# Kernel tuning notes

Hardware: AMD Instinct MI355X
Metric: run time of the kernel (lower is better)

## Reference

```python
import jax, jax.numpy as jnp
import numpy as np

B, S, D, H = 4, 1024, 1024, 16
DK = D // H
BLEND = 0.5
NEG = -1000000000.0


def setup_inputs() -> dict:
    key = jax.random.key(0)
    ks = jax.random.split(key, 16)
    scale = 0.02
    inp = {
        'query': jax.random.normal(ks[0], (B, S, D), jnp.float32),
        'key': jax.random.normal(ks[1], (B, S, D), jnp.float32),
        'value': jax.random.normal(ks[2], (B, S, D), jnp.float32),
        'relation_matrix': jax.random.uniform(ks[3], (B, H, S, S), jnp.float32),
        'Wq': jax.random.normal(ks[4], (D, D), jnp.float32) * scale,
        'bq': jnp.zeros((D,), jnp.float32),
        'Wk': jax.random.normal(ks[5], (D, D), jnp.float32) * scale,
        'bk': jnp.zeros((D,), jnp.float32),
        'Wv': jax.random.normal(ks[6], (D, D), jnp.float32) * scale,
        'bv': jnp.zeros((D,), jnp.float32),
        'Wo': jax.random.normal(ks[7], (D, D), jnp.float32) * scale,
        'bo': jnp.zeros((D,), jnp.float32),
        'mask': jnp.ones((B, 1, S, S), jnp.bool_),
        'padding_mask': jax.random.randint(ks[8], (B, S), 0, 2).astype(jnp.bool_),
    }
    return inp


def _split_heads(x):
    # [B,S,D] -> [B,H,S,DK]
    return x.reshape(B, S, H, DK).transpose(0, 2, 1, 3)


def reference(query, key, value, relation_matrix, Wq, bq, Wk, bk, Wv, bv, Wo, bo, mask, padding_mask):
    q = _split_heads(query @ Wq.T + bq)
    k = _split_heads(key @ Wk.T + bk)
    v = _split_heads(value @ Wv.T + bv)
    # mask * padding_mask (bool AND), broadcast to [B,H,S,S]
    full_mask = mask & padding_mask[:, None, None, :]
    scores = jnp.einsum('bhqd,bhkd->bhqk', q, k) / jnp.sqrt(jnp.float32(DK))
    scores = jnp.where(full_mask, scores, NEG)
    p = jax.nn.softmax(scores, axis=-1)
    p = jnp.where(jnp.isnan(p), jnp.zeros_like(p), p)
    p = BLEND * p + (1.0 - BLEND) * relation_matrix
    p = jnp.where(full_mask, p, 0.0)
    # dropout p=0 -> identity
    x = jnp.einsum('bhqk,bhkd->bhqd', p, v)
    x = x.transpose(0, 2, 1, 3).reshape(B, S, D)
    return x @ Wo.T + bo
```

## Files before the change

kernel.cpp:

```cpp
#include <hip/hip_runtime.h>
#include <hip/hip_bf16.h>

#define B_ 4
#define S_ 1024
#define D_ 1024
#define H_ 16
#define DK_ 64

typedef __attribute__((ext_vector_type(8))) short short8;
typedef __attribute__((ext_vector_type(4))) float f32x4;
typedef unsigned long long ull;

union U16x8 { uint4 q; short8 s; unsigned short h[8]; };

__device__ __forceinline__ unsigned short f2bf(float f) {
  union { float f; unsigned u; } a; a.f = f;
  unsigned u = a.u;
  u += 0x7FFF + ((u >> 16) & 1);
  return (unsigned short)(u >> 16);
}

__device__ __forceinline__ void gload_lds16(const void* g, void* l) {
  __builtin_amdgcn_global_load_lds(
      (const __attribute__((address_space(1))) unsigned int*)g,
      (__attribute__((address_space(3))) unsigned int*)l, 16, 0, 0);
}

__device__ __forceinline__ void fence_sched() {
  asm volatile("" ::: "memory");
}
__device__ __forceinline__ void bar() {
  fence_sched();
  __builtin_amdgcn_s_barrier();
  fence_sched();
}

__global__ void k_prep(const float* __restrict__ q, const float* __restrict__ k,
                       const float* __restrict__ v,
                       const float* __restrict__ Wq, const float* __restrict__ Wk,
                       const float* __restrict__ Wv, const float* __restrict__ Wo,
                       unsigned short* __restrict__ Aq, unsigned short* __restrict__ Ak,
                       unsigned short* __restrict__ Av,
                       unsigned short* __restrict__ WqB, unsigned short* __restrict__ WkB,
                       unsigned short* __restrict__ WvB, unsigned short* __restrict__ WoB,
                       const unsigned char* __restrict__ padraw,
                       ull* __restrict__ qmW) {
  __shared__ unsigned char pl[4096];
  const int b = blockIdx.x, t = threadIdx.x;
  if (b == 8192) {
    bool nonzero_off = false, sawf = false;
    for (int i = 0; i < 128; ++i) {
      unsigned char c = padraw[i];
      if ((i & 3) && c) nonzero_off = true;
      if (c == 0x3F || c == 0x80) sawf = true;
    }
    int fmt = sawf ? 2 : (nonzero_off ? 0 : 1);
    for (int j = 0; j < 16; ++j) {
      int i = t * 16 + j;
      unsigned char val;
      if (fmt == 0)      val = padraw[i] != 0;
      else if (fmt == 1) val = padraw[(size_t)i * 4] != 0;
      else               val = ((const float*)padraw)[i] != 0.f;
      pl[i] = val;
    }
    __syncthreads();
    if (t < 64) {
      int bb = t >> 4, c = t & 15;
      ull m = 0;
      for (int j = 0; j < 64; ++j) m |= (ull)(pl[bb * 1024 + j * 16 + c] & 1) << j;
      qmW[t] = m;
    }
    return;
  }
  const float* src; unsigned short* dst; size_t base;
  if (b < 2048)      { src = q; dst = Aq; base = (size_t)b * 2048; }
  else if (b < 4096) { src = k; dst = Ak; base = (size_t)(b - 2048) * 2048; }
  else if (b < 6144) { src = v; dst = Av; base = (size_t)(b - 4096) * 2048; }
  else {
    int w = (b - 6144) >> 9, bb = (b - 6144) & 511;
    src = w == 0 ? Wq : w == 1 ? Wk : w == 2 ? Wv : Wo;
    dst = w == 0 ? WqB : w == 1 ? WkB : w == 2 ? WvB : WoB;
    base = (size_t)bb * 2048;
  }
  size_t i = base + (size_t)t * 8;
  float4 a = *(const float4*)(src + i);
  float4 c = *(const float4*)(src + i + 4);
  U16x8 o;
  o.h[0]=f2bf(a.x); o.h[1]=f2bf(a.y); o.h[2]=f2bf(a.z); o.h[3]=f2bf(a.w);
  o.h[4]=f2bf(c.x); o.h[5]=f2bf(c.y); o.h[6]=f2bf(c.z); o.h[7]=f2bf(c.w);
  *(uint4*)(dst + i) = o.q;
}

#define BM 128
#define BN 128
#define BKG 64
__global__ __launch_bounds__(256) void k_gemm(
    const unsigned short* __restrict__ A0, const unsigned short* __restrict__ A1,
    const unsigned short* __restrict__ A2,
    const unsigned short* __restrict__ W0, const unsigned short* __restrict__ W1,
    const unsigned short* __restrict__ W2,
    const float* __restrict__ bi0, const float* __restrict__ bi1, const float* __restrict__ bi2,
    void* __restrict__ C0, void* __restrict__ C1, void* __restrict__ C2,
    const ull* __restrict__ qm, int modeSel) {
  __shared__ unsigned short As[2][BM * BKG];
  __shared__ unsigned short Bs[2][BN * BKG];
  const int d0 = blockIdx.x;
  const int chunk = gridDim.x >> 3;
  const int o = (d0 & 7) * chunk + (d0 >> 3);
  const int z = o >> 8;
  const unsigned short* A  = z == 0 ? A0 : z == 1 ? A1 : A2;
  const unsigned short* Bw = z == 0 ? W0 : z == 1 ? W1 : W2;
  const float* bias        = z == 0 ? bi0 : z == 1 ? bi1 : bi2;
  void* Cout               = z == 0 ? C0 : z == 1 ? C1 : C2;
  const int mode = (modeSel == 2) ? 2 : (z == 2 ? 1 : 0);
  const int t = threadIdx.x;
  const int lane = t & 63;
  const int wid = t >> 6;
  const int wm = wid >> 1, wn = wid & 1;
  const int m0 = ((o >> 3) & 31) * BM, n0 = (o & 7) * BN;
  f32x4 acc[4][4] = {};

  auto stage = [&](int kt, int buf) {
    const int k0 = kt * BKG;
    char* AsB = (char*)As[buf]; char* BsB = (char*)Bs[buf];
#pragma unroll
    for (int i = 0; i < 4; ++i) {
      int lx = (t + i * 256) * 16;
      int row = lx >> 7;
      int colb = (lx & 127) ^ ((row & 7) << 4);
      gload_lds16((const char*)A + (size_t)(m0 + row) * (D_ * 2) + k0 * 2 + colb, AsB + lx);
    }
#pragma unroll
    for (int i = 0; i < 4; ++i) {
      int lx = (t + i * 256) * 16;
      int row = lx >> 7;
      int colb = (lx & 127) ^ ((row & 7) << 4);
      gload_lds16((const char*)Bw + (size_t)(n0 + row) * (D_ * 2) + k0 * 2 + colb, BsB + lx);
    }
  };

  asm volatile("s_waitcnt vmcnt(0)" ::: "memory");
  stage(0, 0);
#pragma unroll 1
  for (int kt = 0; kt < D_ / BKG; ++kt) {
    const int cur = kt & 1;
    if (kt < 15) {
      stage(kt + 1, cur ^ 1);
      asm volatile("s_waitcnt vmcnt(8)" ::: "memory");
    } else {
      asm volatile("s_waitcnt vmcnt(0)" ::: "memory");
    }
    __builtin_amdgcn_sched_barrier(0);
    bar();
    char* AsB = (char*)As[cur]; char* BsB = (char*)Bs[cur];
#pragma unroll
    for (int ks = 0; ks < 2; ++ks) {
      short8 aF[4], bF[4];
      int kbyte = ks * 64 + ((lane >> 4) << 4);
#pragma unroll
      for (int m = 0; m < 4; ++m) {
        int row = wm * 64 + m * 16 + (lane & 15);
        U16x8 u; u.q = *(const uint4*)(AsB + row * 128 + (kbyte ^ ((row & 7) << 4)));
        aF[m] = u.s;
      }
#pragma unroll
      for (int n = 0; n < 4; ++n) {
        int row = wn * 64 + n * 16 + (lane & 15);
        U16x8 u; u.q = *(const uint4*)(BsB + row * 128 + (kbyte ^ ((row & 7) << 4)));
        bF[n] = u.s;
      }
#pragma unroll
      for (int m = 0; m < 4; ++m)
#pragma unroll
        for (int n = 0; n < 4; ++n)
          acc[m][n] = __builtin_amdgcn_mfma_f32_16x16x32_bf16(aF[m], bF[n], acc[m][n], 0, 0, 0);
    }
    bar();
  }
#pragma unroll
  for (int m = 0; m < 4; ++m) {
#pragma unroll
    for (int n = 0; n < 4; ++n) {
#pragma unroll
      for (int r = 0; r < 4; ++r) {
        int rg = m0 + wm * 64 + m * 16 + ((lane >> 4) << 2) + r;
        int cg = n0 + wn * 64 + n * 16 + (lane & 15);
        float val = acc[m][n][r] + bias[cg];
        int bb = rg >> 10, s = rg & 1023;
        int hh = cg >> 6, dk = cg & 63;
        if (mode == 0)
          ((unsigned short*)Cout)[((size_t)(bb * H_ + hh) * S_ + s) * DK_ + dk] = f2bf(val);
        else if (mode == 1) {
          float pv = (float)((qm[bb * 16 + (s & 15)] >> (s >> 4)) & 1);
          val *= pv;
          ((unsigned short*)Cout)[((size_t)(bb * H_ + hh) * DK_ + dk) * S_ + s] = f2bf(val);
        } else
          ((float*)Cout)[(size_t)rg * D_ + cg] = val;
      }
    }
  }
}

__global__ __launch_bounds__(256) void k_attn(const unsigned short* __restrict__ Qh,
    const unsigned short* __restrict__ Kh, const unsigned short* __restrict__ Vt,
    const float* __restrict__ rel, const ull* __restrict__ qm,
    unsigned short* __restrict__ Xout) {
  __shared__ unsigned short Ks[2][4096];
  __shared__ unsigned short Vs[2][4096];
  __shared__ float Rl[2][4096];
  __shared__ unsigned short Pl[4096];
  const int t = threadIdx.x, lane = t & 63, wid = t >> 6;
  const int d0 = blockIdx.x;
  const int o = (d0 & 7) * 128 + (d0 >> 3);
  const int qt = o & 15, h = (o >> 4) & 15, b = o >> 8;
  const int bh = b * H_ + h;
  const int c = lane & 15, g = lane >> 4;
  const int q0 = qt * 64 + wid * 16;
  char* PlB = (char*)Pl + wid * 2048;

  ull qmask = qm[b * 16 + c];

  short8 qa[2];
#pragma unroll
  for (int ks = 0; ks < 2; ++ks) {
    U16x8 u;
    u.q = *(const uint4*)((const char*)Qh +
          ((size_t)(bh * S_ + q0 + c) * DK_ + ks * 32 + (g << 3)) * 2);
    qa[ks] = u.s;
  }
  f32x4 eacc[4] = {}, racc[4] = {};
  float Lp[4] = {0.f, 0.f, 0.f, 0.f};

  const char* relblk = (const char*)rel + ((size_t)(bh * S_ + qt * 64) * S_) * 4;
  auto stage = [&](int kt, int buf) {
    const int k0 = kt * 64;
    char* KsB = (char*)Ks[buf];
    char* VsB = (char*)Vs[buf];
    char* RlB = (char*)Rl[buf];
#pragma unroll
    for (int i = 0; i < 2; ++i) {
      int lx = (t + i * 256) * 16;
      int row = lx >> 7;
      int colb = (lx & 127) ^ ((row & 7) << 4);
      gload_lds16((const char*)Kh + ((size_t)(bh * S_ + k0 + row) * DK_) * 2 + colb, KsB + lx);
    }
#pragma unroll
    for (int i = 0; i < 2; ++i) {
      int lx = (t + i * 256) * 16;
      int row = lx >> 7;
      int colb = (lx & 127) ^ ((row & 7) << 4);
      gload_lds16((const char*)Vt + ((size_t)(bh * DK_ + row) * S_ + k0) * 2 + colb, VsB + lx);
    }
#pragma unroll
    for (int i = 0; i < 4; ++i) {
      int lx = t * 16 + i * 4096;
      int row = lx >> 8;
      int inner = (lx & 255) ^ ((row & 7) << 4);
      gload_lds16(relblk + (size_t)row * (S_ * 4) + (size_t)kt * 256 + inner, RlB + lx);
    }
  };

  asm volatile("s_waitcnt vmcnt(0)" ::: "memory");
  stage(0, 0);

#pragma unroll 1
  for (int kt = 0; kt < 16; ++kt) {
    const int cur = kt & 1;
    if (kt < 15) {
      stage(kt + 1, cur ^ 1);
      asm volatile("s_waitcnt vmcnt(8)" ::: "memory");
    } else {
      asm volatile("s_waitcnt vmcnt(0)" ::: "memory");
    }
    __builtin_amdgcn_sched_barrier(0);
    bar();
    char* KsB = (char*)Ks[cur]; char* VsB = (char*)Vs[cur];
    const char* RlB = (const char*)Rl[cur];
#pragma unroll
    for (int kb = 0; kb < 4; ++kb) {
      f32x4 sacc = {};
#pragma unroll
      for (int ks = 0; ks < 2; ++ks) {
        int row = kb * 16 + c;
        int kbyte = ks * 64 + (g << 4);
        U16x8 u; u.q = *(const uint4*)(KsB + row * 128 + (kbyte ^ ((row & 7) << 4)));
        sacc = __builtin_amdgcn_mfma_f32_16x16x32_bf16(qa[ks], u.s, sacc, 0, 0, 0);
      }
      float pv = ((qmask >> (kt * 4 + kb)) & 1) ? 1.0f : 0.0f;
#pragma unroll
      for (int r = 0; r < 4; ++r) {
        float p = __expf(sacc[r] * 0.125f);
        Lp[r] += pv * p;
        int qrow = (g << 2) + r;
        int byteoff = qrow * 128 + (((kb * 16 + c) * 2) ^ ((qrow & 7) << 4));
        *(unsigned short*)(PlB + byteoff) = f2bf(p);
      }
    }
    asm volatile("s_waitcnt lgkmcnt(0)" ::: "memory");
    __builtin_amdgcn_sched_barrier(0);
    short8 pa[2];
#pragma unroll
    for (int ks = 0; ks < 2; ++ks) {
      int kbyte = ks * 64 + (g << 4);
      U16x8 u; u.q = *(const uint4*)(PlB + c * 128 + (kbyte ^ ((c & 7) << 4)));
      pa[ks] = u.s;
    }
    short8 rw[2];
    {
      const int rrow = wid * 16 + c;
      const char* rbase = RlB + rrow * 256;
      const int swz = (c & 7) << 4;
#pragma unroll
      for (int ks = 0; ks < 2; ++ks) {
        int binrow = ks * 128 + (g << 5);
        uint4 f0 = *(const uint4*)(rbase + ((binrow)      ^ swz));
        uint4 f1 = *(const uint4*)(rbase + ((binrow + 16) ^ swz));
        U16x8 w;
        w.h[0]=f2bf(__uint_as_float(f0.x)); w.h[1]=f2bf(__uint_as_float(f0.y));
        w.h[2]=f2bf(__uint_as_float(f0.z)); w.h[3]=f2bf(__uint_as_float(f0.w));
        w.h[4]=f2bf(__uint_as_float(f1.x)); w.h[5]=f2bf(__uint_as_float(f1.y));
        w.h[6]=f2bf(__uint_as_float(f1.z)); w.h[7]=f2bf(__uint_as_float(f1.w));
        rw[ks] = w.s;
      }
    }
#pragma unroll
    for (int nb = 0; nb < 4; ++nb) {
      int row = nb * 16 + c;
      U16x8 u0, u1;
      u0.q = *(const uint4*)(VsB + row * 128 + (((g << 4))      ^ ((row & 7) << 4)));
      u1.q = *(const uint4*)(VsB + row * 128 + ((64 + (g << 4)) ^ ((row & 7) << 4)));
      eacc[nb] = __builtin_amdgcn_mfma_f32_16x16x32_bf16(pa[0],  u0.s, eacc[nb], 0, 0, 0);
      eacc[nb] = __builtin_amdgcn_mfma_f32_16x16x32_bf16(pa[1],  u1.s, eacc[nb], 0, 0, 0);
      racc[nb] = __builtin_amdgcn_mfma_f32_16x16x32_bf16(rw[0],  u0.s, racc[nb], 0, 0, 0);
      racc[nb] = __builtin_amdgcn_mfma_f32_16x16x32_bf16(rw[1],  u1.s, racc[nb], 0, 0, 0);
    }
    bar();
  }
#pragma unroll
  for (int r = 0; r < 4; ++r) {
    float v = Lp[r];
    v += __shfl_xor(v, 1);
    v += __shfl_xor(v, 2);
    v += __shfl_xor(v, 4);
    v += __shfl_xor(v, 8);
    Lp[r] = v;
  }
#pragma unroll
  for (int nb = 0; nb < 4; ++nb) {
#pragma unroll
    for (int r = 0; r < 4; ++r) {
      float invL = Lp[r] > 0.f ? 0.5f / Lp[r] : 0.f;
      float v = eacc[nb][r] * invL + 0.5f * racc[nb][r];
      int srow = q0 + (g << 2) + r;
      int col = h * DK_ + nb * 16 + c;
      Xout[(size_t)(b * S_ + srow) * D_ + col] = f2bf(v);
    }
  }
}

extern "C" void kernel_launch(void* const* d_in, const int* in_sizes, int n_in,
                              void* d_out, int out_size, void* d_ws, size_t ws_size,
                              hipStream_t stream) {
  const float* q   = (const float*)d_in[0];
  const float* k   = (const float*)d_in[1];
  const float* v   = (const float*)d_in[2];
  const float* rel = (const float*)d_in[3];
  const float* Wq  = (const float*)d_in[4];
  const float* bq  = (const float*)d_in[5];
  const float* Wk  = (const float*)d_in[6];
  const float* bk  = (const float*)d_in[7];
  const float* Wv  = (const float*)d_in[8];
  const float* bv  = (const float*)d_in[9];
  const float* Wo  = (const float*)d_in[10];
  const float* bo  = (const float*)d_in[11];
  const unsigned char* padraw = (const unsigned char*)d_in[13];

  char* ws = (char*)d_ws;
  unsigned short* Wqb = (unsigned short*)ws;
  unsigned short* Wkb = Wqb + (1 << 20);
  unsigned short* Wvb = Wkb + (1 << 20);
  unsigned short* Wob = Wvb + (1 << 20);
  unsigned short* Aq  = Wob + (1 << 20);
  unsigned short* Ak  = Aq  + (4 << 20);
  unsigned short* Av  = Ak  + (4 << 20);
  unsigned short* Qh  = Av  + (4 << 20);
  unsigned short* Khd = Qh  + (4 << 20);
  unsigned short* Vtd = Khd + (4 << 20);
  unsigned short* Xa  = Vtd + (4 << 20);
  ull* qmW = (ull*)(Xa + (4 << 20));

  k_prep<<<8193, 256, 0, stream>>>(q, k, v, Wq, Wk, Wv, Wo,
                                   Aq, Ak, Av, Wqb, Wkb, Wvb, Wob,
                                   padraw, qmW);

  k_gemm<<<768, 256, 0, stream>>>(
      Aq, Ak, Av, Wqb, Wkb, Wvb, bq, bk, bv, Qh, Khd, Vtd, qmW, 0);

  k_attn<<<1024, 256, 0, stream>>>(Qh, Khd, Vtd, rel, qmW, Xa);

  k_gemm<<<256, 256, 0, stream>>>(
      Xa, Xa, Xa, Wob, Wob, Wob, bo, bo, bo, d_out, d_out, d_out, qmW, 2);
}
```

Baseline: 211.7 us.

## Restructure attention pipeline to cut LDS footprint with split relation staging

The attention kernel drops double-buffered K and relation tiles. K becomes single-buffered, and the fp32 relation tile is split into two half-tiles (A and B) that are refilled at different points within each key-tile iteration, interleaved with the two halves of the PV MFMA work. This shrinks shared memory per block, likely to raise occupancy, at the cost of more barriers and a less aggressive prefetch distance for K and the relation data. It also replaces the hand-written bf16 rounding with the HIP intrinsic conversion.

```diff
diff --git a/kernel.cpp b/kernel.cpp
--- a/kernel.cpp
+++ b/kernel.cpp
@@ -18,6 +18,12 @@
   unsigned u = a.u;
   u += 0x7FFF + ((u >> 16) & 1);
   return (unsigned short)(u >> 16);
+}
+
+__device__ __forceinline__ unsigned short f2bf_h(float f) {
+  union { __hip_bfloat16 h; unsigned short u; } x;
+  x.h = __float2bfloat16(f);
+  return x.u;
 }
 
 __device__ __forceinline__ void gload_lds16(const void* g, void* l) {
@@ -205,9 +211,10 @@
     const unsigned short* __restrict__ Kh, const unsigned short* __restrict__ Vt,
     const float* __restrict__ rel, const ull* __restrict__ qm,
     unsigned short* __restrict__ Xout) {
-  __shared__ unsigned short Ks[2][4096];
+  __shared__ unsigned short Ks[4096];
   __shared__ unsigned short Vs[2][4096];
-  __shared__ float Rl[2][4096];
+  __shared__ float RlA[2048];
+  __shared__ float RlB[2048];
   __shared__ unsigned short Pl[4096];
   const int t = threadIdx.x, lane = t & 63, wid = t >> 6;
   const int d0 = blockIdx.x;
@@ -232,11 +239,8 @@
   float Lp[4] = {0.f, 0.f, 0.f, 0.f};
 
   const char* relblk = (const char*)rel + ((size_t)(bh * S_ + qt * 64) * S_) * 4;
-  auto stage = [&](int kt, int buf) {
-    const int k0 = kt * 64;
-    char* KsB = (char*)Ks[buf];
-    char* VsB = (char*)Vs[buf];
-    char* RlB = (char*)Rl[buf];
+  auto stageK = [&](int kt) {
+    char* KsB = (char*)Ks; const int k0 = kt * 64;
 #pragma unroll
     for (int i = 0; i < 2; ++i) {
       int lx = (t + i * 256) * 16;
@@ -244,6 +248,9 @@
       int colb = (lx & 127) ^ ((row & 7) << 4);
       gload_lds16((const char*)Kh + ((size_t)(bh * S_ + k0 + row) * DK_) * 2 + colb, KsB + lx);
     }
+  };
+  auto stageV = [&](int kt, int buf) {
+    char* VsB = (char*)Vs[buf]; const int k0 = kt * 64;
 #pragma unroll
     for (int i = 0; i < 2; ++i) {
       int lx = (t + i * 256) * 16;
@@ -251,31 +258,52 @@
       int colb = (lx & 127) ^ ((row & 7) << 4);
       gload_lds16((const char*)Vt + ((size_t)(bh * DK_ + row) * S_ + k0) * 2 + colb, VsB + lx);
     }
-#pragma unroll
-    for (int i = 0; i < 4; ++i) {
+  };
+  auto stageRelA = [&](int kt) {
+    char* R = (char*)RlA;
+#pragma unroll
+    for (int i = 0; i < 2; ++i) {
       int lx = t * 16 + i * 4096;
-      int row = lx >> 8;
-      int inner = (lx & 255) ^ ((row & 7) << 4);
-      gload_lds16(relblk + (size_t)row * (S_ * 4) + (size_t)kt * 256 + inner, RlB + lx);
-    }
+      int row = lx >> 7;
+      int inner = (lx & 127) ^ ((row & 7) << 4);
+      gload_lds16(relblk + (size_t)row * (S_ * 4) + (size_t)kt * 256 + inner, R + lx);
+    }
+  };
+  auto stageRelB = [&](int kt) {
+    char* R = (char*)RlB;
+#pragma unroll
+    for (int i = 0; i < 2; ++i) {
+      int lx = t * 16 + i * 4096;
+      int row = lx >> 7;
+      int inner = (lx & 127) ^ ((row & 7) << 4);
+      gload_lds16(relblk + (size_t)row * (S_ * 4) + (size_t)kt * 256 + 128 + inner, R + lx);
+    }
+  };
+  const int rrow = wid * 16 + c;
+  const int rsw = (rrow & 7) << 4;
+  auto relfrag = [&](const char* Rbase) -> short8 {
+    const char* rb = Rbase + rrow * 128;
+    uint4 f0 = *(const uint4*)(rb + ((g * 32)      ^ rsw));
+    uint4 f1 = *(const uint4*)(rb + ((g * 32 + 16) ^ rsw));
+    U16x8 w;
+    w.h[0]=f2bf_h(__uint_as_float(f0.x)); w.h[1]=f2bf_h(__uint_as_float(f0.y));
+    w.h[2]=f2bf_h(__uint_as_float(f0.z)); w.h[3]=f2bf_h(__uint_as_float(f0.w));
+    w.h[4]=f2bf_h(__uint_as_float(f1.x)); w.h[5]=f2bf_h(__uint_as_float(f1.y));
+    w.h[6]=f2bf_h(__uint_as_float(f1.z)); w.h[7]=f2bf_h(__uint_as_float(f1.w));
+    return w.s;
   };
 
   asm volatile("s_waitcnt vmcnt(0)" ::: "memory");
-  stage(0, 0);
+  stageK(0); stageV(0, 0); stageRelA(0);
+  stageRelB(0);
 
 #pragma unroll 1
   for (int kt = 0; kt < 16; ++kt) {
     const int cur = kt & 1;
-    if (kt < 15) {
-      stage(kt + 1, cur ^ 1);
-      asm volatile("s_waitcnt vmcnt(8)" ::: "memory");
-    } else {
-      asm volatile("s_waitcnt vmcnt(0)" ::: "memory");
-    }
+    asm volatile("s_waitcnt vmcnt(2)" ::: "memory");
     __builtin_amdgcn_sched_barrier(0);
     bar();
-    char* KsB = (char*)Ks[cur]; char* VsB = (char*)Vs[cur];
-    const char* RlB = (const char*)Rl[cur];
+    char* KsB = (char*)Ks; char* VsB = (char*)Vs[cur];
 #pragma unroll
     for (int kb = 0; kb < 4; ++kb) {
       f32x4 sacc = {};
@@ -293,7 +321,7 @@
         Lp[r] += pv * p;
         int qrow = (g << 2) + r;
         int byteoff = qrow * 128 + (((kb * 16 + c) * 2) ^ ((qrow & 7) << 4));
-        *(unsigned short*)(PlB + byteoff) = f2bf(p);
+        *(unsigned short*)(PlB + byteoff) = f2bf_h(p);
       }
     }
     asm volatile("s_waitcnt lgkmcnt(0)" ::: "memory");
@@ -305,36 +333,37 @@
       U16x8 u; u.q = *(const uint4*)(PlB + c * 128 + (kbyte ^ ((c & 7) << 4)));
       pa[ks] = u.s;
     }
-    short8 rw[2];
-    {
-      const int rrow = wid * 16 + c;
-      const char* rbase = RlB + rrow * 256;
-      const int swz = (c & 7) << 4;
-#pragma unroll
-      for (int ks = 0; ks < 2; ++ks) {
-        int binrow = ks * 128 + (g << 5);
-        uint4 f0 = *(const uint4*)(rbase + ((binrow)      ^ swz));
-        uint4 f1 = *(const uint4*)(rbase + ((binrow + 16) ^ swz));
-        U16x8 w;
-        w.h[0]=f2bf(__uint_as_float(f0.x)); w.h[1]=f2bf(__uint_as_float(f0.y));
-        w.h[2]=f2bf(__uint_as_float(f0.z)); w.h[3]=f2bf(__uint_as_float(f0.w));
-        w.h[4]=f2bf(__uint_as_float(f1.x)); w.h[5]=f2bf(__uint_as_float(f1.y));
-        w.h[6]=f2bf(__uint_as_float(f1.z)); w.h[7]=f2bf(__uint_as_float(f1.w));
-        rw[ks] = w.s;
-      }
-    }
+    short8 rwA = relfrag((const char*)RlA);
 #pragma unroll
     for (int nb = 0; nb < 4; ++nb) {
       int row = nb * 16 + c;
-      U16x8 u0, u1;
-      u0.q = *(const uint4*)(VsB + row * 128 + (((g << 4))      ^ ((row & 7) << 4)));
+      U16x8 u0;
+      u0.q = *(const uint4*)(VsB + row * 128 + (((g << 4)) ^ ((row & 7) << 4)));
+      eacc[nb] = __builtin_amdgcn_mfma_f32_16x16x32_bf16(pa[0], u0.s, eacc[nb], 0, 0, 0);
+      racc[nb] = __builtin_amdgcn_mfma_f32_16x16x32_bf16(rwA,   u0.s, racc[nb], 0, 0, 0);
+    }
+    bar();
+    if (kt < 15) {
+      stageK(kt + 1);
+      stageV(kt + 1, cur ^ 1);
+      stageRelA(kt + 1);
+      asm volatile("s_waitcnt vmcnt(6)" ::: "memory");
+    } else {
+      asm volatile("s_waitcnt vmcnt(0)" ::: "memory");
+    }
+    __builtin_amdgcn_sched_barrier(0);
+    bar();
+    short8 rwB = relfrag((const char*)RlB);
+#pragma unroll
+    for (int nb = 0; nb < 4; ++nb) {
+      int row = nb * 16 + c;
+      U16x8 u1;
       u1.q = *(const uint4*)(VsB + row * 128 + ((64 + (g << 4)) ^ ((row & 7) << 4)));
-      eacc[nb] = __builtin_amdgcn_mfma_f32_16x16x32_bf16(pa[0],  u0.s, eacc[nb], 0, 0, 0);
-      eacc[nb] = __builtin_amdgcn_mfma_f32_16x16x32_bf16(pa[1],  u1.s, eacc[nb], 0, 0, 0);
-      racc[nb] = __builtin_amdgcn_mfma_f32_16x16x32_bf16(rw[0],  u0.s, racc[nb], 0, 0, 0);
-      racc[nb] = __builtin_amdgcn_mfma_f32_16x16x32_bf16(rw[1],  u1.s, racc[nb], 0, 0, 0);
-    }
-    bar();
+      eacc[nb] = __builtin_amdgcn_mfma_f32_16x16x32_bf16(pa[1], u1.s, eacc[nb], 0, 0, 0);
+      racc[nb] = __builtin_amdgcn_mfma_f32_16x16x32_bf16(rwB,   u1.s, racc[nb], 0, 0, 0);
+    }
+    bar();
+    if (kt < 15) stageRelB(kt + 1);
   }
 #pragma unroll
   for (int r = 0; r < 4; ++r) {
@@ -353,7 +382,7 @@
       float v = eacc[nb][r] * invL + 0.5f * racc[nb][r];
       int srow = q0 + (g << 2) + r;
       int col = h * DK_ + nb * 16 + c;
-      Xout[(size_t)(b * S_ + srow) * D_ + col] = f2bf(v);
+      Xout[(size_t)(b * S_ + srow) * D_ + col] = f2bf_h(v);
     }
   }
 }
```

Measured after the change: 231.3 us. 1.09x slower.
